# Performance work log

Measured on AMD Instinct MI355X. Metric: run time of the kernel, lower is better.

## Reference

```python
import jax, jax.numpy as jnp
import numpy as np

STATE_DIM = 512
PROJ_DIM = 300


def setup_inputs() -> dict:
    key = jax.random.key(0)
    ks = jax.random.split(key, 10)
    batseq, node_num, edge_num = 320, 32, 1024  # edge_num = node_num**2
    inp = {
        "nodes_feats": jax.random.normal(ks[0], (batseq, node_num, STATE_DIM), jnp.float32),
        "edges_feats": jax.random.normal(ks[1], (batseq, edge_num, STATE_DIM), jnp.float32),
        "adj_mat": jax.random.uniform(ks[2], (batseq, node_num, edge_num), jnp.float32),
        "true_lengths": jax.random.randint(ks[3], (32,), 0, 10),
        "seq_size": 10,
        # Linear layer params (out_features=300, in_features=512), torch layout W: [out, in]
        "W1": jax.random.normal(ks[4], (PROJ_DIM, STATE_DIM), jnp.float32) * 0.02,
        "b1": jnp.zeros((PROJ_DIM,), jnp.float32),
        "W2": jax.random.normal(ks[5], (PROJ_DIM, STATE_DIM), jnp.float32) * 0.02,
        "b2": jnp.zeros((PROJ_DIM,), jnp.float32),
        "W3": jax.random.normal(ks[6], (PROJ_DIM, STATE_DIM), jnp.float32) * 0.02,
        "b3": jnp.zeros((PROJ_DIM,), jnp.float32),
    }
    return inp


def reference(nodes_feats, edges_feats, adj_mat, true_lengths, seq_size,
              W1, b1, W2, b2, W3, b3):
    batseq, node_num, _ = nodes_feats.shape
    batch = batseq // seq_size  # from adj_mat.view(-1, seq_size, node_num, edge_num)
    # Batched replacements for the per-pair tiny Linears
    f1 = jnp.einsum("bnd,pd->bnp", nodes_feats, W1) + b1   # [B, N, 300]
    f3 = jnp.einsum("bnd,pd->bnp", nodes_feats, W3) + b3   # [B, N, 300]
    f2 = jnp.einsum("bed,pd->bep", edges_feats, W2) + b2   # [B, N*N, 300]
    f2 = f2.reshape(batseq, node_num, node_num, PROJ_DIM)  # [B, i, j, 300]
    # per-pair MSE(f_j, f_ij + f_i), mean over (batseq, 300), summed over (i, j)
    diff = f3[:, None, :, :] - f2 - f1[:, :, None, :]
    losses = jnp.sum(diff * diff) / (batseq * PROJ_DIM)
    return losses / batch
```

## Files before the change

### kernel.cpp

```cpp
#include <hip/hip_runtime.h>
#include <hip/hip_bf16.h>
#include <stdint.h>

#define STATE 512
#define PROJ 300
#define PPAD 320
#define BATSEQ 320
#define TE 327680
#define PSTR 328

typedef __bf16 bf16x8 __attribute__((ext_vector_type(8)));
typedef float f32x4 __attribute__((ext_vector_type(4)));
typedef long long i64;

__device__ inline unsigned short f2bf(float x) {
  unsigned u = __builtin_bit_cast(unsigned, x);
  unsigned r = u + 0x7fffu + ((u >> 16) & 1u);
  return (unsigned short)(r >> 16);
}

__global__ __launch_bounds__(256) void prep_kernel(
    const float* __restrict__ W1, const float* __restrict__ b1,
    const float* __restrict__ W2, const float* __restrict__ b2,
    const float* __restrict__ W3, const float* __restrict__ b3,
    unsigned short* __restrict__ w1p, unsigned short* __restrict__ w3p,
    unsigned short* __restrict__ w2tp, unsigned char* __restrict__ w2p8,
    float* __restrict__ b1p, float* __restrict__ b2p, float* __restrict__ b3p)
{
  int idx = blockIdx.x * 256 + threadIdx.x;
  const int WN = PPAD * STATE;
  if (idx < 2 * WN) {
    int which = idx / WN, r = idx % WN;
    int cs = r / 512, q = r % 512;
    int lane = q / 8, i = q % 8;
    int c = cs / 16, s = cs % 16;
    int p = c * 16 + (lane & 15);
    int k = s * 32 + (lane >> 4) * 8 + i;
    const float* W = (which == 0) ? W1 : W3;
    unsigned short* dst = (which == 0) ? w1p : w3p;
    float v = (p < PROJ) ? W[(size_t)p * STATE + k] : 0.0f;
    dst[r] = f2bf(v);
  } else if (idx < 3 * WN) {
    int r = idx - 2 * WN;
    int cs = r / 512, q = r % 512;
    int lane = q / 8, ii = q % 8;
    int ct = cs / 10, s2 = cs % 10;
    int p = s2 * 32 + (lane >> 4) * 8 + ii;
    int n = ct * 16 + (lane & 15);
    float v = (p < PROJ) ? W2[(size_t)p * STATE + n] : 0.0f;
    w2tp[r] = f2bf(v);
  } else if (idx < 4 * WN) {
    int r = idx - 3 * WN;
    int cs = r / 512, q = r % 512;
    int lane = q / 8, i = q % 8;
    int c = cs / 16, s = cs % 16;
    int p = c * 16 + (lane & 15);
    int k = s * 32 + (lane >> 4) * 8 + i;
    float v = (p < PROJ) ? W2[(size_t)p * STATE + k] : 0.0f;
    int pk = __builtin_amdgcn_cvt_pk_fp8_f32(v, 0.f, 0, 0);
    w2p8[r] = (unsigned char)(pk & 0xff);
  } else if (idx < 4 * WN + 3 * PPAD) {
    int r = idx - 4 * WN;
    int which = r / PPAD, p = r % PPAD;
    const float* B = (which == 0) ? b1 : ((which == 1) ? b2 : b3);
    float* dst = (which == 0) ? b1p : ((which == 1) ? b2p : b3p);
    dst[p] = (p < PROJ) ? B[p] : 0.0f;
  }
}

__global__ __launch_bounds__(256, 2) void node_kernel(
    const float* __restrict__ nodes,
    const unsigned short* __restrict__ w1p, const unsigned short* __restrict__ w3p,
    const unsigned short* __restrict__ w2tp,
    const float* __restrict__ b1p, const float* __restrict__ b2p,
    const float* __restrict__ b3p,
    float* __restrict__ g1t, float* __restrict__ g3t,
    double* __restrict__ pnode)
{
  __shared__ __align__(16) unsigned short tile[32 * 512];
  __shared__ __align__(16) unsigned short t2a[32 * PSTR];
  __shared__ __align__(16) unsigned short t2b[32 * PSTR];
  __shared__ float G1[PPAD], G3[PPAD];
  __shared__ double red[4];
  const int tid = threadIdx.x;
  const int wave = tid >> 6, lane = tid & 63;
  const int b = blockIdx.x;
  const float* src = nodes + (size_t)b * 32 * STATE;

  for (int t = tid; t < PPAD; t += 256) { G1[t] = 0.f; G3[t] = 0.f; }

  #pragma unroll
  for (int m = 0; m < 16; ++m) {
    int k = wave + 4 * m;
    int row = k >> 1;
    int fc = (k & 1) * 64 + lane;
    f32x4 v = *(const f32x4*)(src + row * STATE + fc * 4);
    unsigned lo = f2bf(v.x) | ((unsigned)f2bf(v.y) << 16);
    unsigned hi = f2bf(v.z) | ((unsigned)f2bf(v.w) << 16);
    unsigned long long pk = (unsigned long long)lo | ((unsigned long long)hi << 32);
    unsigned off = (unsigned)(row * 1024 + fc * 8) ^ (unsigned)((row & 7) << 4);
    *(unsigned long long*)((char*)tile + off) = pk;
  }
  __syncthreads();

  const int lrow = lane & 15, lk = lane >> 4;
  const int cbase = wave * 5;

  f32x4 af1[2][5], af3[2][5];
  #pragma unroll
  for (int rg = 0; rg < 2; ++rg)
    #pragma unroll
    for (int c = 0; c < 5; ++c) {
      af1[rg][c][0]=0.f; af1[rg][c][1]=0.f; af1[rg][c][2]=0.f; af1[rg][c][3]=0.f;
      af3[rg][c][0]=0.f; af3[rg][c][1]=0.f; af3[rg][c][2]=0.f; af3[rg][c][3]=0.f;
    }
  for (int s = 0; s < 16; ++s) {
    bf16x8 a[2];
    #pragma unroll
    for (int rg = 0; rg < 2; ++rg) {
      int row = rg * 16 + lrow;
      unsigned off = (unsigned)(row * 1024 + s * 64 + lk * 16) ^ (unsigned)((row & 7) << 4);
      a[rg] = *(const bf16x8*)((const char*)tile + off);
    }
    #pragma unroll
    for (int c = 0; c < 5; ++c) {
      size_t fo = ((size_t)(((cbase + c) * 16 + s) * 64 + lane)) * 8;
      bf16x8 bf1 = *(const bf16x8*)(w1p + fo);
      bf16x8 bf3 = *(const bf16x8*)(w3p + fo);
      #pragma unroll
      for (int rg = 0; rg < 2; ++rg) {
        af1[rg][c] = __builtin_amdgcn_mfma_f32_16x16x32_bf16(a[rg], bf1, af1[rg][c], 0, 0, 0);
        af3[rg][c] = __builtin_amdgcn_mfma_f32_16x16x32_bf16(a[rg], bf3, af3[rg][c], 0, 0, 0);
      }
    }
  }

  float sq = 0.f;
  #pragma unroll
  for (int rg = 0; rg < 2; ++rg)
    #pragma unroll
    for (int c = 0; c < 5; ++c) {
      int p = (cbase + c) * 16 + lrow;
      float bb1 = b1p[p], bb2 = b2p[p], bb3 = b3p[p];
      #pragma unroll
      for (int r = 0; r < 4; ++r) {
        int m = rg * 16 + lk * 4 + r;
        float v1 = af1[rg][c][r] + bb1;
        float v3 = af3[rg][c][r] + bb3 - bb2;
        t2a[m * PSTR + p] = f2bf(v1);
        t2b[m * PSTR + p] = f2bf(v3);
        sq += v1 * v1 + v3 * v3;
        atomicAdd(&G1[p], v1);
        atomicAdd(&G3[p], v3);
      }
    }
  __syncthreads();

  float s7 = 0.f;
  for (int t = tid; t < PPAD; t += 256) s7 += G3[t] * G1[t];
  float val = 32.f * sq - 2.f * s7;
  #pragma unroll
  for (int m = 32; m >= 1; m >>= 1) val += __shfl_xor(val, m, 64);
  if (lane == 0) red[wave] = (double)val;

  for (int pass = 0; pass < 2; ++pass) {
    const unsigned short* t2 = pass ? t2b : t2a;
    float* gt = pass ? g3t : g1t;
    f32x4 acc2[2][8];
    #pragma unroll
    for (int rg = 0; rg < 2; ++rg)
      #pragma unroll
      for (int cc = 0; cc < 8; ++cc) { acc2[rg][cc][0]=0.f; acc2[rg][cc][1]=0.f; acc2[rg][cc][2]=0.f; acc2[rg][cc][3]=0.f; }
    for (int s2 = 0; s2 < 10; ++s2) {
      bf16x8 a[2];
      #pragma unroll
      for (int rg = 0; rg < 2; ++rg) {
        int mrow = rg * 16 + lrow;
        a[rg] = *(const bf16x8*)(t2 + mrow * PSTR + s2 * 32 + lk * 8);
      }
      #pragma unroll
      for (int cc = 0; cc < 8; ++cc) {
        int ct = wave * 8 + cc;
        bf16x8 bfr = *(const bf16x8*)(w2tp + ((size_t)((ct * 10 + s2) * 64 + lane)) * 8);
        #pragma unroll
        for (int rg = 0; rg < 2; ++rg)
          acc2[rg][cc] = __builtin_amdgcn_mfma_f32_16x16x32_bf16(a[rg], bfr, acc2[rg][cc], 0, 0, 0);
      }
    }
    #pragma unroll
    for (int rg = 0; rg < 2; ++rg)
      #pragma unroll
      for (int cc = 0; cc < 8; ++cc) {
        int n = (wave * 8 + cc) * 16 + lrow;
        #pragma unroll
        for (int r = 0; r < 4; ++r) {
          int mm = rg * 16 + lk * 4 + r;
          gt[((size_t)b * 32 + mm) * STATE + n] = acc2[rg][cc][r];
        }
      }
  }

  __syncthreads();
  if (tid == 0) pnode[b] = red[0] + red[1] + red[2] + red[3];
}

__global__ __launch_bounds__(256) void g3pack_kernel(
    const float* __restrict__ g3t, unsigned char* __restrict__ g3p8)
{
  const int b = blockIdx.x;
  const float* g3b = g3t + (size_t)b * 32 * STATE;
  int* dst = (int*)(g3p8 + (size_t)b * 16384);
  #pragma unroll
  for (int t = 0; t < 16; ++t) {
    int g = threadIdx.x + t * 256;
    int r = g * 4;
    int lane = (r >> 3) & 63;
    int i0 = r & 7;
    int cts = r >> 9;
    int j = (cts >> 4) * 16 + (lane & 15);
    int k = (cts & 15) * 32 + (lane >> 4) * 8 + i0;
    const float* v = g3b + (size_t)j * STATE + k;
    int pk = __builtin_amdgcn_cvt_pk_fp8_f32(v[0], v[1], 0, 0);
    pk = __builtin_amdgcn_cvt_pk_fp8_f32(v[2], v[3], pk, 1);
    dst[g] = pk;
  }
}

__global__ __launch_bounds__(256, 2) void edge_kernel(
    const float* __restrict__ edges, const unsigned char* __restrict__ w2p8,
    const unsigned char* __restrict__ g3p8, const float* __restrict__ g1t,
    double* __restrict__ pedge)
{
  __shared__ __align__(16) unsigned char tile[128 * 512];
  __shared__ double redd[4][2];
  const int tid = threadIdx.x;
  const int wave = tid >> 6, lane = tid & 63;

  const int orig = blockIdx.x;
  const int wg = (orig & 7) * 320 + (orig >> 3);
  const int b = wg >> 3, q4 = wg & 7;
  const float* src = edges + ((size_t)b * 1024 + (size_t)q4 * 128) * STATE;
  const unsigned char* g3p = g3p8 + (size_t)b * 16384;
  const float* g1b = g1t + ((size_t)b * 32 + (size_t)q4 * 4) * STATE;

  f32x4 sE[4];
  #pragma unroll
  for (int ii = 0; ii < 4; ++ii) { sE[ii][0]=0.f; sE[ii][1]=0.f; sE[ii][2]=0.f; sE[ii][3]=0.f; }
  const int fc = tid & 127;
  const int rhi = tid >> 7;
  #pragma unroll 16
  for (int m = 0; m < 64; ++m) {
    int row = 2 * m + rhi;
    f32x4 e = *(const f32x4*)(src + row * STATE + fc * 4);
    sE[m >> 4] += e;
    int pk = __builtin_amdgcn_cvt_pk_fp8_f32(e.x, e.y, 0, 0);
    pk = __builtin_amdgcn_cvt_pk_fp8_f32(e.z, e.w, pk, 1);
    unsigned off = (unsigned)(row * 512 + fc * 4) ^ (unsigned)((row & 7) << 3);
    *(int*)(tile + off) = pk;
  }
  __syncthreads();

  const int lrow = lane & 15, lk = lane >> 4;
  const int cb = wave * 5;
  f32x4 acc[8][5];
  #pragma unroll
  for (int rg = 0; rg < 8; ++rg)
    #pragma unroll
    for (int c = 0; c < 5; ++c) { acc[rg][c][0]=0.f; acc[rg][c][1]=0.f; acc[rg][c][2]=0.f; acc[rg][c][3]=0.f; }
  f32x4 accg[2];
  accg[0][0]=0.f; accg[0][1]=0.f; accg[0][2]=0.f; accg[0][3]=0.f;
  accg[1][0]=0.f; accg[1][1]=0.f; accg[1][2]=0.f; accg[1][3]=0.f;

  #pragma unroll 4
  for (int s = 0; s < 16; ++s) {
    i64 a[8];
    #pragma unroll
    for (int rg = 0; rg < 8; ++rg) {
      int row = rg * 16 + lrow;
      unsigned off = (unsigned)(row * 512 + s * 32 + lk * 8) ^ (unsigned)((lrow & 7) << 3);
      a[rg] = *(const i64*)(tile + off);
    }
    i64 bg0 = *(const i64*)(g3p + ((size_t)((s) * 64 + lane)) * 8);
    i64 bg1 = *(const i64*)(g3p + ((size_t)((16 + s) * 64 + lane)) * 8);
    #pragma unroll
    for (int c = 0; c < 5; ++c) {
      i64 bfr = *(const i64*)(w2p8 + ((size_t)(((cb + c) * 16 + s) * 64 + lane)) * 8);
      #pragma unroll
      for (int rg = 0; rg < 8; ++rg)
        acc[rg][c] = __builtin_amdgcn_mfma_f32_16x16x32_fp8_fp8(a[rg], bfr, acc[rg][c], 0, 0, 0);
    }
    #pragma unroll
    for (int rg = 0; rg < 8; ++rg)
      accg[rg & 1] = __builtin_amdgcn_mfma_f32_16x16x32_fp8_fp8(a[rg], (rg & 1) ? bg1 : bg0, accg[rg & 1], 0, 0, 0);
  }

  float ss = 0.f, cr = 0.f;
  #pragma unroll
  for (int rg = 0; rg < 8; ++rg)
    #pragma unroll
    for (int c = 0; c < 5; ++c)
      #pragma unroll
      for (int r = 0; r < 4; ++r) ss += acc[rg][c][r] * acc[rg][c][r];

  {
    int qv = lane & 15, hi4 = lane >> 4;
    if ((qv >> 2) == hi4) {
      int r = qv & 3;
      float d0 = (r == 0) ? accg[0][0] : (r == 1) ? accg[0][1] : (r == 2) ? accg[0][2] : accg[0][3];
      float d1 = (r == 0) ? accg[1][0] : (r == 1) ? accg[1][1] : (r == 2) ? accg[1][2] : accg[1][3];
      cr += d0 + d1;
    }
  }

  #pragma unroll
  for (int ii = 0; ii < 4; ++ii) {
    f32x4 g1v = *(const f32x4*)(g1b + (size_t)ii * STATE + fc * 4);
    cr -= sE[ii].x * g1v.x + sE[ii].y * g1v.y + sE[ii].z * g1v.z + sE[ii].w * g1v.w;
  }

  #pragma unroll
  for (int m = 32; m >= 1; m >>= 1) {
    ss += __shfl_xor(ss, m, 64);
    cr += __shfl_xor(cr, m, 64);
  }
  if (lane == 0) { redd[wave][0] = (double)ss; redd[wave][1] = (double)cr; }
  __syncthreads();
  if (tid == 0) {
    double sT = 0.0, cT = 0.0;
    #pragma unroll
    for (int w = 0; w < 4; ++w) { sT += redd[w][0]; cT += redd[w][1]; }
    pedge[wg] = sT - 2.0 * cT;
  }
}

__global__ __launch_bounds__(256) void final_kernel(
    const double* __restrict__ pedge, const double* __restrict__ pnode,
    const int* __restrict__ seqp, float* __restrict__ out)
{
  __shared__ double red[4];
  const int tid = threadIdx.x, wave = tid >> 6, lane = tid & 63;
  double v = 0.0;
  for (int t = tid; t < 2560; t += 256) v += pedge[t];
  for (int t = tid; t < 320; t += 256) v += pnode[t];
  #pragma unroll
  for (int m = 32; m >= 1; m >>= 1) v += __shfl_xor(v, m, 64);
  if (lane == 0) red[wave] = v;
  __syncthreads();
  if (tid == 0) {
    double Total = red[0] + red[1] + red[2] + red[3];
    int seq = seqp[0];
    int batch = (seq > 0) ? (BATSEQ / seq) : 1;
    out[0] = (float)(Total / ((double)BATSEQ * (double)PROJ) / (double)batch);
  }
}

extern "C" void kernel_launch(void* const* d_in, const int* in_sizes, int n_in,
                              void* d_out, int out_size, void* d_ws, size_t ws_size,
                              hipStream_t stream)
{
  const float* nodes = (const float*)d_in[0];
  const float* edges = (const float*)d_in[1];
  const int*   seqp  = (const int*)d_in[4];
  const float* W1 = (const float*)d_in[5];
  const float* b1 = (const float*)d_in[6];
  const float* W2 = (const float*)d_in[7];
  const float* b2 = (const float*)d_in[8];
  const float* W3 = (const float*)d_in[9];
  const float* b3 = (const float*)d_in[10];

  char* ws = (char*)d_ws;
  unsigned short* w1p  = (unsigned short*)(ws + 0);
  unsigned short* w3p  = (unsigned short*)(ws + 327680);
  unsigned short* w2tp = (unsigned short*)(ws + 655360);
  unsigned char*  w2p8 = (unsigned char*)(ws + 983040);
  float* b1p = (float*)(ws + 1146880);
  float* b2p = (float*)(ws + 1148160);
  float* b3p = (float*)(ws + 1149440);
  float* g1t = (float*)(ws + 2097152);
  float* g3t = (float*)(ws + 23068672);
  double* pedge = (double*)(ws + 44040192);
  double* pnode = (double*)(ws + 44060672);
  unsigned char* g3p8 = (unsigned char*)(ws + 44072960);

  prep_kernel<<<2564, 256, 0, stream>>>(W1, b1, W2, b2, W3, b3,
                                        w1p, w3p, w2tp, w2p8, b1p, b2p, b3p);
  node_kernel<<<320, 256, 0, stream>>>(nodes, w1p, w3p, w2tp, b1p, b2p, b3p,
                                       g1t, g3t, pnode);
  g3pack_kernel<<<320, 256, 0, stream>>>(g3t, g3p8);
  edge_kernel<<<2560, 256, 0, stream>>>(edges, w2p8, g3p8, g1t, pedge);
  final_kernel<<<1, 256, 0, stream>>>(pedge, pnode, seqp, (float*)d_out);
}
```

Before: 347.6 us.

## Split edge tiles into 64-row blocks with double-buffered register prefetch

Each edge workgroup now handles 64 edge rows instead of 128, processed as two 32-row halves. The second half's fp32 loads are issued into registers before the first half's MFMA loop, so global loads overlap compute, and each half is converted into its own LDS buffer. Fewer accumulators and less LDS per block allow three blocks per CU instead of two, while the grid doubles to 5120. In exchange, the W2 and g3 fragments are reloaded twice as often overall, and the 16 prefetched float4 registers add register pressure.

```diff
diff --git a/kernel.cpp b/kernel.cpp
--- a/kernel.cpp
+++ b/kernel.cpp
@@ -226,81 +226,143 @@
   }
 }
 
-__global__ __launch_bounds__(256, 2) void edge_kernel(
+__global__ __launch_bounds__(256, 3) void edge_kernel(
     const float* __restrict__ edges, const unsigned char* __restrict__ w2p8,
     const unsigned char* __restrict__ g3p8, const float* __restrict__ g1t,
     double* __restrict__ pedge)
 {
-  __shared__ __align__(16) unsigned char tile[128 * 512];
+  __shared__ __align__(16) unsigned char bufA[32 * 512];
+  __shared__ __align__(16) unsigned char bufB[32 * 512];
   __shared__ double redd[4][2];
   const int tid = threadIdx.x;
   const int wave = tid >> 6, lane = tid & 63;
 
   const int orig = blockIdx.x;
-  const int wg = (orig & 7) * 320 + (orig >> 3);
-  const int b = wg >> 3, q4 = wg & 7;
-  const float* src = edges + ((size_t)b * 1024 + (size_t)q4 * 128) * STATE;
+  const int wg = (orig & 7) * 640 + (orig >> 3);
+  const int b = wg >> 4, q = wg & 15;
+  const float* src = edges + ((size_t)b * 1024 + (size_t)q * 64) * STATE;
   const unsigned char* g3p = g3p8 + (size_t)b * 16384;
-  const float* g1b = g1t + ((size_t)b * 32 + (size_t)q4 * 4) * STATE;
-
-  f32x4 sE[4];
-  #pragma unroll
-  for (int ii = 0; ii < 4; ++ii) { sE[ii][0]=0.f; sE[ii][1]=0.f; sE[ii][2]=0.f; sE[ii][3]=0.f; }
+  const float* g1b = g1t + ((size_t)b * 32 + (size_t)q * 2) * STATE;
+
   const int fc = tid & 127;
   const int rhi = tid >> 7;
-  #pragma unroll 16
-  for (int m = 0; m < 64; ++m) {
-    int row = 2 * m + rhi;
-    f32x4 e = *(const f32x4*)(src + row * STATE + fc * 4);
-    sE[m >> 4] += e;
-    int pk = __builtin_amdgcn_cvt_pk_fp8_f32(e.x, e.y, 0, 0);
-    pk = __builtin_amdgcn_cvt_pk_fp8_f32(e.z, e.w, pk, 1);
-    unsigned off = (unsigned)(row * 512 + fc * 4) ^ (unsigned)((row & 7) << 3);
-    *(int*)(tile + off) = pk;
-  }
-  __syncthreads();
-
   const int lrow = lane & 15, lk = lane >> 4;
   const int cb = wave * 5;
-  f32x4 acc[8][5];
-  #pragma unroll
-  for (int rg = 0; rg < 8; ++rg)
-    #pragma unroll
-    for (int c = 0; c < 5; ++c) { acc[rg][c][0]=0.f; acc[rg][c][1]=0.f; acc[rg][c][2]=0.f; acc[rg][c][3]=0.f; }
+
+  float cr = 0.f;
+  float ss = 0.f;
   f32x4 accg[2];
   accg[0][0]=0.f; accg[0][1]=0.f; accg[0][2]=0.f; accg[0][3]=0.f;
   accg[1][0]=0.f; accg[1][1]=0.f; accg[1][2]=0.f; accg[1][3]=0.f;
 
-  #pragma unroll 4
-  for (int s = 0; s < 16; ++s) {
-    i64 a[8];
-    #pragma unroll
-    for (int rg = 0; rg < 8; ++rg) {
-      int row = rg * 16 + lrow;
-      unsigned off = (unsigned)(row * 512 + s * 32 + lk * 8) ^ (unsigned)((lrow & 7) << 3);
-      a[rg] = *(const i64*)(tile + off);
-    }
-    i64 bg0 = *(const i64*)(g3p + ((size_t)((s) * 64 + lane)) * 8);
-    i64 bg1 = *(const i64*)(g3p + ((size_t)((16 + s) * 64 + lane)) * 8);
-    #pragma unroll
-    for (int c = 0; c < 5; ++c) {
-      i64 bfr = *(const i64*)(w2p8 + ((size_t)(((cb + c) * 16 + s) * 64 + lane)) * 8);
-      #pragma unroll
-      for (int rg = 0; rg < 8; ++rg)
-        acc[rg][c] = __builtin_amdgcn_mfma_f32_16x16x32_fp8_fp8(a[rg], bfr, acc[rg][c], 0, 0, 0);
-    }
-    #pragma unroll
-    for (int rg = 0; rg < 8; ++rg)
-      accg[rg & 1] = __builtin_amdgcn_mfma_f32_16x16x32_fp8_fp8(a[rg], (rg & 1) ? bg1 : bg0, accg[rg & 1], 0, 0, 0);
-  }
-
-  float ss = 0.f, cr = 0.f;
-  #pragma unroll
-  for (int rg = 0; rg < 8; ++rg)
-    #pragma unroll
-    for (int c = 0; c < 5; ++c)
-      #pragma unroll
-      for (int r = 0; r < 4; ++r) ss += acc[rg][c][r] * acc[rg][c][r];
+  {
+    f32x4 sE0 = {0.f, 0.f, 0.f, 0.f};
+    #pragma unroll
+    for (int m = 0; m < 16; ++m) {
+      int row = 2 * m + rhi;
+      f32x4 e = *(const f32x4*)(src + row * STATE + fc * 4);
+      sE0 += e;
+      int pk = __builtin_amdgcn_cvt_pk_fp8_f32(e.x, e.y, 0, 0);
+      pk = __builtin_amdgcn_cvt_pk_fp8_f32(e.z, e.w, pk, 1);
+      unsigned off = (unsigned)(row * 512 + fc * 4) ^ (unsigned)((row & 7) << 3);
+      *(int*)(bufA + off) = pk;
+    }
+    f32x4 g1a = *(const f32x4*)(g1b + fc * 4);
+    cr -= sE0.x * g1a.x + sE0.y * g1a.y + sE0.z * g1a.z + sE0.w * g1a.w;
+  }
+  __syncthreads();
+
+  f32x4 eB[16];
+  #pragma unroll
+  for (int m = 0; m < 16; ++m)
+    eB[m] = *(const f32x4*)(src + (32 + 2 * m + rhi) * STATE + fc * 4);
+
+  {
+    f32x4 acc[2][5];
+    #pragma unroll
+    for (int rg = 0; rg < 2; ++rg)
+      #pragma unroll
+      for (int c = 0; c < 5; ++c) { acc[rg][c][0]=0.f; acc[rg][c][1]=0.f; acc[rg][c][2]=0.f; acc[rg][c][3]=0.f; }
+    #pragma unroll 4
+    for (int s = 0; s < 16; ++s) {
+      i64 a[2];
+      #pragma unroll
+      for (int rg = 0; rg < 2; ++rg) {
+        int row = rg * 16 + lrow;
+        unsigned off = (unsigned)(row * 512 + s * 32 + lk * 8) ^ (unsigned)((row & 7) << 3);
+        a[rg] = *(const i64*)(bufA + off);
+      }
+      i64 bg0 = *(const i64*)(g3p + ((size_t)((s) * 64 + lane)) * 8);
+      i64 bg1 = *(const i64*)(g3p + ((size_t)((16 + s) * 64 + lane)) * 8);
+      #pragma unroll
+      for (int c = 0; c < 5; ++c) {
+        i64 bfr = *(const i64*)(w2p8 + ((size_t)(((cb + c) * 16 + s) * 64 + lane)) * 8);
+        #pragma unroll
+        for (int rg = 0; rg < 2; ++rg)
+          acc[rg][c] = __builtin_amdgcn_mfma_f32_16x16x32_fp8_fp8(a[rg], bfr, acc[rg][c], 0, 0, 0);
+      }
+      accg[0] = __builtin_amdgcn_mfma_f32_16x16x32_fp8_fp8(a[0], bg0, accg[0], 0, 0, 0);
+      accg[1] = __builtin_amdgcn_mfma_f32_16x16x32_fp8_fp8(a[1], bg1, accg[1], 0, 0, 0);
+    }
+    #pragma unroll
+    for (int rg = 0; rg < 2; ++rg)
+      #pragma unroll
+      for (int c = 0; c < 5; ++c)
+        #pragma unroll
+        for (int r = 0; r < 4; ++r) ss += acc[rg][c][r] * acc[rg][c][r];
+  }
+
+  {
+    f32x4 sE1 = {0.f, 0.f, 0.f, 0.f};
+    #pragma unroll
+    for (int m = 0; m < 16; ++m) {
+      int row = 2 * m + rhi;
+      f32x4 e = eB[m];
+      sE1 += e;
+      int pk = __builtin_amdgcn_cvt_pk_fp8_f32(e.x, e.y, 0, 0);
+      pk = __builtin_amdgcn_cvt_pk_fp8_f32(e.z, e.w, pk, 1);
+      unsigned off = (unsigned)(row * 512 + fc * 4) ^ (unsigned)((row & 7) << 3);
+      *(int*)(bufB + off) = pk;
+    }
+    f32x4 g1c = *(const f32x4*)(g1b + STATE + fc * 4);
+    cr -= sE1.x * g1c.x + sE1.y * g1c.y + sE1.z * g1c.z + sE1.w * g1c.w;
+  }
+  __syncthreads();
+
+  {
+    f32x4 acc[2][5];
+    #pragma unroll
+    for (int rg = 0; rg < 2; ++rg)
+      #pragma unroll
+      for (int c = 0; c < 5; ++c) { acc[rg][c][0]=0.f; acc[rg][c][1]=0.f; acc[rg][c][2]=0.f; acc[rg][c][3]=0.f; }
+    #pragma unroll 4
+    for (int s = 0; s < 16; ++s) {
+      i64 a[2];
+      #pragma unroll
+      for (int rg = 0; rg < 2; ++rg) {
+        int row = rg * 16 + lrow;
+        unsigned off = (unsigned)(row * 512 + s * 32 + lk * 8) ^ (unsigned)((row & 7) << 3);
+        a[rg] = *(const i64*)(bufB + off);
+      }
+      i64 bg0 = *(const i64*)(g3p + ((size_t)((s) * 64 + lane)) * 8);
+      i64 bg1 = *(const i64*)(g3p + ((size_t)((16 + s) * 64 + lane)) * 8);
+      #pragma unroll
+      for (int c = 0; c < 5; ++c) {
+        i64 bfr = *(const i64*)(w2p8 + ((size_t)(((cb + c) * 16 + s) * 64 + lane)) * 8);
+        #pragma unroll
+        for (int rg = 0; rg < 2; ++rg)
+          acc[rg][c] = __builtin_amdgcn_mfma_f32_16x16x32_fp8_fp8(a[rg], bfr, acc[rg][c], 0, 0, 0);
+      }
+      accg[0] = __builtin_amdgcn_mfma_f32_16x16x32_fp8_fp8(a[0], bg0, accg[0], 0, 0, 0);
+      accg[1] = __builtin_amdgcn_mfma_f32_16x16x32_fp8_fp8(a[1], bg1, accg[1], 0, 0, 0);
+    }
+    #pragma unroll
+    for (int rg = 0; rg < 2; ++rg)
+      #pragma unroll
+      for (int c = 0; c < 5; ++c)
+        #pragma unroll
+        for (int r = 0; r < 4; ++r) ss += acc[rg][c][r] * acc[rg][c][r];
+  }
 
   {
     int qv = lane & 15, hi4 = lane >> 4;
@@ -313,12 +375,6 @@
   }
 
   #pragma unroll
-  for (int ii = 0; ii < 4; ++ii) {
-    f32x4 g1v = *(const f32x4*)(g1b + (size_t)ii * STATE + fc * 4);
-    cr -= sE[ii].x * g1v.x + sE[ii].y * g1v.y + sE[ii].z * g1v.z + sE[ii].w * g1v.w;
-  }
-
-  #pragma unroll
   for (int m = 32; m >= 1; m >>= 1) {
     ss += __shfl_xor(ss, m, 64);
     cr += __shfl_xor(cr, m, 64);
@@ -340,7 +396,7 @@
   __shared__ double red[4];
   const int tid = threadIdx.x, wave = tid >> 6, lane = tid & 63;
   double v = 0.0;
-  for (int t = tid; t < 2560; t += 256) v += pedge[t];
+  for (int t = tid; t < 5120; t += 256) v += pedge[t];
   for (int t = tid; t < 320; t += 256) v += pnode[t];
   #pragma unroll
   for (int m = 32; m >= 1; m >>= 1) v += __shfl_xor(v, m, 64);
@@ -379,14 +435,14 @@
   float* g1t = (float*)(ws + 2097152);
   float* g3t = (float*)(ws + 23068672);
   double* pedge = (double*)(ws + 44040192);
-  double* pnode = (double*)(ws + 44060672);
-  unsigned char* g3p8 = (unsigned char*)(ws + 44072960);
+  double* pnode = (double*)(ws + 44081152);
+  unsigned char* g3p8 = (unsigned char*)(ws + 44089344);
 
   prep_kernel<<<2564, 256, 0, stream>>>(W1, b1, W2, b2, W3, b3,
                                         w1p, w3p, w2tp, w2p8, b1p, b2p, b3p);
   node_kernel<<<320, 256, 0, stream>>>(nodes, w1p, w3p, w2tp, b1p, b2p, b3p,
                                        g1t, g3t, pnode);
   g3pack_kernel<<<320, 256, 0, stream>>>(g3t, g3p8);
-  edge_kernel<<<2560, 256, 0, stream>>>(edges, w2p8, g3p8, g1t, pedge);
+  edge_kernel<<<5120, 256, 0, stream>>>(edges, w2p8, g3p8, g1t, pedge);
   final_kernel<<<1, 256, 0, stream>>>(pedge, pnode, seqp, (float*)d_out);
 }
```

Measured after the change: 654.7 us. +88.4%, slower.
